# Performance work log

Measured on AMD Instinct MI355X. Metric: run time of the kernel, lower is better.

Reference implementation:

```python
import jax, jax.numpy as jnp
import numpy as np

NEG_FILL = -10000000.0  # matches torch masked_fill value


def setup_inputs() -> dict:
    key = jax.random.key(0)
    kq, kk, kv = jax.random.split(key, 3)
    B, H, S, D = 4, 16, 2048, 64
    Q = jax.random.normal(kq, (B, H, S, D), dtype=jnp.float32)
    K = jax.random.normal(kk, (B, H, S, D), dtype=jnp.float32)
    V = jax.random.normal(kv, (B, H, S, D), dtype=jnp.float32)
    return {"Q": Q, "K": K, "V": V}


def reference(Q, K, V):
    # Q,K,V: [B,H,S,D]
    D = K.shape[-1]
    scale = 1.0 / jnp.sqrt(jnp.asarray(D, dtype=Q.dtype))
    # scores: [B,H,S,S]
    scores = jnp.einsum("bhqd,bhkd->bhqk", Q, K) * scale
    S = scores.shape[-1]
    # causal mask: True above diagonal (future positions) -> filled with NEG_FILL
    causal = jnp.triu(jnp.ones((S, S), dtype=bool), k=1)
    scores = jnp.where(causal, jnp.asarray(NEG_FILL, dtype=scores.dtype), scores)
    attn = jax.nn.softmax(scores, axis=-1)
    return jnp.einsum("bhqk,bhkd->bhqd", attn, V)
```

## Files before the change

### kernel.cpp

```cpp
#include <hip/hip_runtime.h>
#include <hip/hip_bf16.h>


#define SEQ 2048
#define DIM 64
#define BH  64

typedef _Float16 half8  __attribute__((ext_vector_type(8)));
typedef _Float16 half4v __attribute__((ext_vector_type(4)));
typedef float    float4v __attribute__((ext_vector_type(4)));

__device__ __forceinline__ void async16(const _Float16* g, _Float16* l) {
    __builtin_amdgcn_global_load_lds(
        (const __attribute__((address_space(1))) void*)g,
        (__attribute__((address_space(3))) void*)l, 16, 0, 0);
}

__global__ __launch_bounds__(256)
void prep_kernel(const float* __restrict__ K, const float* __restrict__ V,
                 _Float16* __restrict__ Kh, _Float16* __restrict__ Vt) {
    const int bid = blockIdx.x;
    const int tid = threadIdx.x;
    if (bid < 4096) {
        size_t idx = (size_t)bid * 2048 + (size_t)tid * 8;
        float4v a = *(const float4v*)(K + idx);
        float4v b = *(const float4v*)(K + idx + 4);
        half8 h;
        h[0] = (_Float16)a[0]; h[1] = (_Float16)a[1];
        h[2] = (_Float16)a[2]; h[3] = (_Float16)a[3];
        h[4] = (_Float16)b[0]; h[5] = (_Float16)b[1];
        h[6] = (_Float16)b[2]; h[7] = (_Float16)b[3];
        *(half8*)(Kh + idx) = h;
    } else {
        const int b  = bid - 4096;
        const int bh = b >> 5;
        const int s0 = (b & 31) * 64;
        const int dg = tid >> 4;
        const int sg = tid & 15;
        const float* vp = V + ((size_t)bh * SEQ + s0 + sg * 4) * DIM + dg * 4;
        float4v r0 = *(const float4v*)(vp);
        float4v r1 = *(const float4v*)(vp + DIM);
        float4v r2 = *(const float4v*)(vp + 2 * DIM);
        float4v r3 = *(const float4v*)(vp + 3 * DIM);
#pragma unroll
        for (int dd = 0; dd < 4; ++dd) {
            half4v w;
            w[0] = (_Float16)r0[dd]; w[1] = (_Float16)r1[dd];
            w[2] = (_Float16)r2[dd]; w[3] = (_Float16)r3[dd];
            *(half4v*)(Vt + ((size_t)bh * DIM + dg * 4 + dd) * SEQ + s0 + sg * 4) = w;
        }
    }
}

__global__ __launch_bounds__(256, 4)
void fa_main(const float* __restrict__ Q, const _Float16* __restrict__ Kh,
             const _Float16* __restrict__ Vt, float* __restrict__ O) {
    const int bid = blockIdx.x;
    const int bh  = bid >> 4;
    const int pr  = bid & 15;

    const float*    Qb = Q  + (size_t)bh * SEQ * DIM;
    const _Float16* Kb = Kh + (size_t)bh * SEQ * DIM;
    const _Float16* Vb = Vt + (size_t)bh * DIM * SEQ;
    float*          Ob = O  + (size_t)bh * SEQ * DIM;

    const int tid  = threadIdx.x;
    const int wave = tid >> 6;
    const int lane = tid & 63;
    const int row  = lane & 15;
    const int quad = lane >> 4;

    __shared__ _Float16 Kl[2][64 * 64];
    __shared__ _Float16 Vl[2][64 * 64];
    __shared__ _Float16 Pl[4][16 * 64];

    const float SC = 0.125f * 1.44269504f;

#define STAGE(bsel, kt_)                                                        \
    {                                                                           \
        const _Float16* Kt0 = Kb + (size_t)(kt_) * 64 * DIM;                    \
        const _Float16* Vt0 = Vb + (size_t)(kt_) * 64;                          \
        _Pragma("unroll")                                                       \
        for (int i = 0; i < 2; ++i) {                                           \
            int pos = wave * 128 + i * 64 + lane;                               \
            int rr  = pos >> 3;                                                 \
            int cc  = (pos & 7) ^ (rr & 7);                                     \
            async16(Kt0 + (size_t)rr * DIM + cc * 8,                            \
                    &Kl[bsel][0] + (size_t)(wave * 128 + i * 64) * 8);          \
            async16(Vt0 + (size_t)rr * SEQ + cc * 8,                            \
                    &Vl[bsel][0] + (size_t)(wave * 128 + i * 64) * 8);          \
        }                                                                       \
    }

    for (int ph = 0; ph < 2; ++ph) {
        const int qt = ph ? (31 - pr) : pr;
        const int q0 = qt * 64;

        half8 qf[2];
        {
            const float* qp = Qb + (size_t)(q0 + wave * 16 + row) * DIM;
#pragma unroll
            for (int s = 0; s < 2; ++s) {
                const float* p = qp + s * 32 + quad * 8;
                float4v a = *(const float4v*)p;
                float4v b = *(const float4v*)(p + 4);
                half8 h;
                h[0] = (_Float16)(a[0] * SC); h[1] = (_Float16)(a[1] * SC);
                h[2] = (_Float16)(a[2] * SC); h[3] = (_Float16)(a[3] * SC);
                h[4] = (_Float16)(b[0] * SC); h[5] = (_Float16)(b[1] * SC);
                h[6] = (_Float16)(b[2] * SC); h[7] = (_Float16)(b[3] * SC);
                qf[s] = h;
            }
        }

        float l_part = 0.f;
        float4v o_acc[4];
#pragma unroll
        for (int c = 0; c < 4; ++c) { float4v z = {0.f, 0.f, 0.f, 0.f}; o_acc[c] = z; }

        STAGE(0, 0)
        __syncthreads();

        for (int kt = 0; kt <= qt; ++kt) {
            const int cb = kt & 1;
            if (kt < qt) STAGE(cb ^ 1, kt + 1)

            float4v sacc[4];
#pragma unroll
            for (int c = 0; c < 4; ++c) { float4v z = {0.f, 0.f, 0.f, 0.f}; sacc[c] = z; }
#pragma unroll
            for (int c = 0; c < 4; ++c) {
                const int kv = c * 16 + row;
#pragma unroll
                for (int s = 0; s < 2; ++s) {
                    const int ch = (s * 4 + quad) ^ (kv & 7);
                    half8 kf = *(const half8*)&Kl[cb][kv * 64 + ch * 8];
                    sacc[c] = __builtin_amdgcn_mfma_f32_16x16x32_f16(kf, qf[s], sacc[c], 0, 0, 0);
                }
            }

            float pv[4][4];
            if (kt == qt) {
                const int ql = wave * 16 + row;
#pragma unroll
                for (int c = 0; c < 4; ++c)
#pragma unroll
                    for (int r = 0; r < 4; ++r) {
                        int kvl = c * 16 + quad * 4 + r;
                        float sx = (kvl > ql) ? -1e30f : sacc[c][r];
                        float p  = exp2f(fminf(sx, 14.f));
                        pv[c][r] = p;
                        l_part  += p;
                    }
            } else {
#pragma unroll
                for (int c = 0; c < 4; ++c)
#pragma unroll
                    for (int r = 0; r < 4; ++r) {
                        float p = exp2f(fminf(sacc[c][r], 14.f));
                        pv[c][r] = p;
                        l_part += p;
                    }
            }

#pragma unroll
            for (int c = 0; c < 4; ++c) {
                half4v w;
                w[0] = (_Float16)pv[c][0]; w[1] = (_Float16)pv[c][1];
                w[2] = (_Float16)pv[c][2]; w[3] = (_Float16)pv[c][3];
                const int jc = c * 2 + (quad >> 1);
                const int col = ((jc ^ (row & 7)) << 3) + (quad & 1) * 4;
                *(half4v*)&Pl[wave][row * 64 + col] = w;
            }
            asm volatile("s_waitcnt lgkmcnt(0)" ::: "memory");
            half8 af[2];
#pragma unroll
            for (int s = 0; s < 2; ++s) {
                const int js = (s * 4 + quad) ^ (row & 7);
                af[s] = *(const half8*)&Pl[wave][row * 64 + js * 8];
            }

#pragma unroll
            for (int c = 0; c < 4; ++c) {
                const int d = c * 16 + row;
#pragma unroll
                for (int s = 0; s < 2; ++s) {
                    const int ch = (s * 4 + quad) ^ (d & 7);
                    half8 vf = *(const half8*)&Vl[cb][d * 64 + ch * 8];
                    o_acc[c] = __builtin_amdgcn_mfma_f32_16x16x32_f16(vf, af[s], o_acc[c], 0, 0, 0);
                }
            }

            __syncthreads();
        }

        float l = l_part;
        l += __shfl_xor(l, 16);
        l += __shfl_xor(l, 32);
        const float inv = 1.0f / l;
        float* op = Ob + (size_t)(q0 + wave * 16 + row) * DIM + quad * 4;
#pragma unroll
        for (int c = 0; c < 4; ++c) {
            float4v o;
            o[0] = o_acc[c][0] * inv; o[1] = o_acc[c][1] * inv;
            o[2] = o_acc[c][2] * inv; o[3] = o_acc[c][3] * inv;
            *(float4v*)(op + c * 16) = o;
        }
    }
}

__global__ __launch_bounds__(256)
void fa_causal_fallback(const float* __restrict__ Q, const float* __restrict__ K,
                        const float* __restrict__ V, float* __restrict__ O) {
    const int bid = blockIdx.x;
    const int bh  = bid >> 5;
    const int qt  = bid & 31;
    const int q0  = qt * 64;

    const float* Qb = Q + (size_t)bh * SEQ * DIM;
    const float* Kb = K + (size_t)bh * SEQ * DIM;
    const float* Vb = V + (size_t)bh * SEQ * DIM;
    float*       Ob = O + (size_t)bh * SEQ * DIM;

    const int tid  = threadIdx.x;
    const int wave = tid >> 6;
    const int lane = tid & 63;
    const int row  = lane & 15;
    const int quad = lane >> 4;

    __shared__ _Float16 Kl[64][72];
    __shared__ _Float16 Vt[64][72];
    __shared__ _Float16 Pl[4][16][72];

    half8 qf[2];
    {
        const float* qp = Qb + (size_t)(q0 + wave * 16 + row) * DIM;
#pragma unroll
        for (int s = 0; s < 2; ++s) {
            const float* p = qp + s * 32 + quad * 8;
            float4v a = *(const float4v*)p;
            float4v b = *(const float4v*)(p + 4);
            half8 h;
            h[0] = (_Float16)a[0]; h[1] = (_Float16)a[1];
            h[2] = (_Float16)a[2]; h[3] = (_Float16)a[3];
            h[4] = (_Float16)b[0]; h[5] = (_Float16)b[1];
            h[6] = (_Float16)b[2]; h[7] = (_Float16)b[3];
            qf[s] = h;
        }
    }

    float m_i[4] = {-1e30f, -1e30f, -1e30f, -1e30f};
    float l_i[4] = {0.f, 0.f, 0.f, 0.f};
    float4v o_acc[4];
#pragma unroll
    for (int c = 0; c < 4; ++c) { float4v z = {0.f, 0.f, 0.f, 0.f}; o_acc[c] = z; }

    const float LOG2E = 1.44269504f;

    for (int kt = 0; kt <= qt; ++kt) {
        __syncthreads();
        {
            const int kvr = tid >> 2;
            const int c4  = tid & 3;
            const float* kp = Kb + (size_t)(kt * 64 + kvr) * DIM + c4 * 16;
            const float* vp = Vb + (size_t)(kt * 64 + kvr) * DIM + c4 * 16;
#pragma unroll
            for (int i = 0; i < 4; ++i) {
                float4v kx = *(const float4v*)(kp + i * 4);
                float4v vx = *(const float4v*)(vp + i * 4);
#pragma unroll
                for (int j = 0; j < 4; ++j) {
                    Kl[kvr][c4 * 16 + i * 4 + j] = (_Float16)kx[j];
                    Vt[c4 * 16 + i * 4 + j][kvr] = (_Float16)vx[j];
                }
            }
        }
        __syncthreads();

        float4v sacc[4];
#pragma unroll
        for (int c = 0; c < 4; ++c) { float4v z = {0.f, 0.f, 0.f, 0.f}; sacc[c] = z; }
#pragma unroll
        for (int c = 0; c < 4; ++c)
#pragma unroll
            for (int s = 0; s < 2; ++s) {
                half8 kf = *(const half8*)&Kl[c * 16 + row][s * 32 + quad * 8];
                sacc[c] = __builtin_amdgcn_mfma_f32_16x16x32_f16(qf[s], kf, sacc[c], 0, 0, 0);
            }

        float sv[4][4];
        const bool diag = (kt == qt);
#pragma unroll
        for (int c = 0; c < 4; ++c)
#pragma unroll
            for (int r = 0; r < 4; ++r) {
                float v = sacc[c][r] * 0.125f;
                if (diag) {
                    int kvl = c * 16 + row;
                    int ql  = wave * 16 + quad * 4 + r;
                    if (kvl > ql) v = -1e30f;
                }
                sv[c][r] = v;
            }

        float mnew[4], alpha[4];
#pragma unroll
        for (int r = 0; r < 4; ++r) {
            float rm = fmaxf(fmaxf(sv[0][r], sv[1][r]), fmaxf(sv[2][r], sv[3][r]));
            rm = fmaxf(rm, __shfl_xor(rm, 1));
            rm = fmaxf(rm, __shfl_xor(rm, 2));
            rm = fmaxf(rm, __shfl_xor(rm, 4));
            rm = fmaxf(rm, __shfl_xor(rm, 8));
            mnew[r]  = fmaxf(m_i[r], rm);
            alpha[r] = exp2f((m_i[r] - mnew[r]) * LOG2E);
            m_i[r]   = mnew[r];
        }
        float rs[4] = {0.f, 0.f, 0.f, 0.f};
#pragma unroll
        for (int c = 0; c < 4; ++c)
#pragma unroll
            for (int r = 0; r < 4; ++r) {
                float p = exp2f((sv[c][r] - mnew[r]) * LOG2E);
                sv[c][r] = p;
                rs[r] += p;
            }
#pragma unroll
        for (int r = 0; r < 4; ++r) {
            float s = rs[r];
            s += __shfl_xor(s, 1);
            s += __shfl_xor(s, 2);
            s += __shfl_xor(s, 4);
            s += __shfl_xor(s, 8);
            l_i[r] = l_i[r] * alpha[r] + s;
        }
#pragma unroll
        for (int c = 0; c < 4; ++c)
#pragma unroll
            for (int r = 0; r < 4; ++r)
                o_acc[c][r] *= alpha[r];

#pragma unroll
        for (int c = 0; c < 4; ++c)
#pragma unroll
            for (int r = 0; r < 4; ++r)
                Pl[wave][quad * 4 + r][c * 16 + row] = (_Float16)sv[c][r];
        __syncthreads();

        half8 af[2];
#pragma unroll
        for (int s = 0; s < 2; ++s)
            af[s] = *(const half8*)&Pl[wave][row][s * 32 + quad * 8];
#pragma unroll
        for (int c = 0; c < 4; ++c)
#pragma unroll
            for (int s = 0; s < 2; ++s) {
                half8 vf = *(const half8*)&Vt[c * 16 + row][s * 32 + quad * 8];
                o_acc[c] = __builtin_amdgcn_mfma_f32_16x16x32_f16(af[s], vf, o_acc[c], 0, 0, 0);
            }
    }

#pragma unroll
    for (int r = 0; r < 4; ++r) {
        float inv = 1.0f / l_i[r];
        float* op = Ob + (size_t)(q0 + wave * 16 + quad * 4 + r) * DIM;
#pragma unroll
        for (int c = 0; c < 4; ++c)
            op[c * 16 + row] = o_acc[c][r] * inv;
    }
}

extern "C" void kernel_launch(void* const* d_in, const int* in_sizes, int n_in,
                              void* d_out, int out_size, void* d_ws, size_t ws_size,
                              hipStream_t stream) {
    const float* Q = (const float*)d_in[0];
    const float* K = (const float*)d_in[1];
    const float* V = (const float*)d_in[2];
    float* O = (float*)d_out;

    const size_t elems = (size_t)BH * SEQ * DIM;
    const size_t need  = 2 * elems * sizeof(_Float16);

    if (ws_size >= need) {
        _Float16* Kh = (_Float16*)d_ws;
        _Float16* Vt = Kh + elems;
        prep_kernel<<<4096 + 2048, 256, 0, stream>>>(K, V, Kh, Vt);
        fa_main<<<BH * 16, 256, 0, stream>>>(Q, Kh, Vt, O);
    } else {
        fa_causal_fallback<<<BH * 32, 256, 0, stream>>>(Q, K, V, O);
    }
}
```

Before: 209.3 us.

## Transpose V through swizzled LDS in prep and remap blocks across XCDs

The V transpose in the prep kernel now loads rows coalesced into a swizzled shared-memory tile, then writes 16-byte transposed chunks. Before, it wrote scattered 8-byte stores. The main kernel's block index is remapped so all query tiles of a batch-head land on the same XCD, which should improve L2 reuse of K/V. The QK MFMA chain also starts from a zero constant instead of explicitly zeroed accumulators. The cost is an extra LDS round trip and a barrier in prep.

```diff
diff --git a/kernel.cpp b/kernel.cpp
--- a/kernel.cpp
+++ b/kernel.cpp
@@ -32,22 +32,49 @@
         h[6] = (_Float16)b[2]; h[7] = (_Float16)b[3];
         *(half8*)(Kh + idx) = h;
     } else {
+        __shared__ _Float16 Vl[64 * 64];
         const int b  = bid - 4096;
         const int bh = b >> 5;
         const int s0 = (b & 31) * 64;
-        const int dg = tid >> 4;
-        const int sg = tid & 15;
-        const float* vp = V + ((size_t)bh * SEQ + s0 + sg * 4) * DIM + dg * 4;
-        float4v r0 = *(const float4v*)(vp);
-        float4v r1 = *(const float4v*)(vp + DIM);
-        float4v r2 = *(const float4v*)(vp + 2 * DIM);
-        float4v r3 = *(const float4v*)(vp + 3 * DIM);
-#pragma unroll
-        for (int dd = 0; dd < 4; ++dd) {
-            half4v w;
-            w[0] = (_Float16)r0[dd]; w[1] = (_Float16)r1[dd];
-            w[2] = (_Float16)r2[dd]; w[3] = (_Float16)r3[dd];
-            *(half4v*)(Vt + ((size_t)bh * DIM + dg * 4 + dd) * SEQ + s0 + sg * 4) = w;
+        {
+            const int r   = tid >> 2;
+            const int c16 = (tid & 3) * 16;
+            const float* p = V + ((size_t)bh * SEQ + s0 + r) * DIM + c16;
+            float4v x0 = *(const float4v*)(p);
+            float4v x1 = *(const float4v*)(p + 4);
+            float4v x2 = *(const float4v*)(p + 8);
+            float4v x3 = *(const float4v*)(p + 12);
+            half8 h0, h1;
+            h0[0] = (_Float16)x0[0]; h0[1] = (_Float16)x0[1];
+            h0[2] = (_Float16)x0[2]; h0[3] = (_Float16)x0[3];
+            h0[4] = (_Float16)x1[0]; h0[5] = (_Float16)x1[1];
+            h0[6] = (_Float16)x1[2]; h0[7] = (_Float16)x1[3];
+            h1[0] = (_Float16)x2[0]; h1[1] = (_Float16)x2[1];
+            h1[2] = (_Float16)x2[2]; h1[3] = (_Float16)x2[3];
+            h1[4] = (_Float16)x3[0]; h1[5] = (_Float16)x3[1];
+            h1[6] = (_Float16)x3[2]; h1[7] = (_Float16)x3[3];
+            const int k  = (r + (r >> 3)) & 7;
+            const int j0 = c16 >> 3;
+            *(half8*)&Vl[r * 64 + ((j0    ) ^ k) * 8] = h0;
+            *(half8*)&Vl[r * 64 + ((j0 + 1) ^ k) * 8] = h1;
+        }
+        __syncthreads();
+        {
+            const int d  = tid >> 2;
+            const int sc = (tid & 3) * 16;
+            const int dh = d >> 3;
+            const int dl = d & 7;
+            half8 o0, o1;
+#pragma unroll
+            for (int j = 0; j < 8; ++j) {
+                const int s1 = sc + j;
+                const int s2 = sc + 8 + j;
+                o0[j] = Vl[s1 * 64 + ((dh ^ ((s1 + (s1 >> 3)) & 7)) << 3) + dl];
+                o1[j] = Vl[s2 * 64 + ((dh ^ ((s2 + (s2 >> 3)) & 7)) << 3) + dl];
+            }
+            _Float16* op = Vt + ((size_t)bh * DIM + d) * SEQ + s0 + sc;
+            *(half8*)op       = o0;
+            *(half8*)(op + 8) = o1;
         }
     }
 }
@@ -56,8 +83,10 @@
 void fa_main(const float* __restrict__ Q, const _Float16* __restrict__ Kh,
              const _Float16* __restrict__ Vt, float* __restrict__ O) {
     const int bid = blockIdx.x;
-    const int bh  = bid >> 4;
-    const int pr  = bid & 15;
+    const int xcd = bid & 7;
+    const int m   = bid >> 3;
+    const int pr  = m & 15;
+    const int bh  = xcd * 8 + (m >> 4);
 
     const float*    Qb = Q  + (size_t)bh * SEQ * DIM;
     const _Float16* Kb = Kh + (size_t)bh * SEQ * DIM;
@@ -75,6 +104,7 @@
     __shared__ _Float16 Pl[4][16 * 64];
 
     const float SC = 0.125f * 1.44269504f;
+    const float4v z0 = {0.f, 0.f, 0.f, 0.f};
 
 #define STAGE(bsel, kt_)                                                        \
     {                                                                           \
@@ -127,16 +157,14 @@
 
             float4v sacc[4];
 #pragma unroll
-            for (int c = 0; c < 4; ++c) { float4v z = {0.f, 0.f, 0.f, 0.f}; sacc[c] = z; }
-#pragma unroll
             for (int c = 0; c < 4; ++c) {
-                const int kv = c * 16 + row;
-#pragma unroll
-                for (int s = 0; s < 2; ++s) {
-                    const int ch = (s * 4 + quad) ^ (kv & 7);
-                    half8 kf = *(const half8*)&Kl[cb][kv * 64 + ch * 8];
-                    sacc[c] = __builtin_amdgcn_mfma_f32_16x16x32_f16(kf, qf[s], sacc[c], 0, 0, 0);
-                }
+                const int kv  = c * 16 + row;
+                const int ch0 = quad ^ (kv & 7);
+                const int ch1 = (4 + quad) ^ (kv & 7);
+                half8 kf0 = *(const half8*)&Kl[cb][kv * 64 + ch0 * 8];
+                half8 kf1 = *(const half8*)&Kl[cb][kv * 64 + ch1 * 8];
+                float4v s = __builtin_amdgcn_mfma_f32_16x16x32_f16(kf0, qf[0], z0, 0, 0, 0);
+                sacc[c]   = __builtin_amdgcn_mfma_f32_16x16x32_f16(kf1, qf[1], s, 0, 0, 0);
             }
 
             float pv[4][4];
@@ -168,7 +196,7 @@
                 half4v w;
                 w[0] = (_Float16)pv[c][0]; w[1] = (_Float16)pv[c][1];
                 w[2] = (_Float16)pv[c][2]; w[3] = (_Float16)pv[c][3];
-                const int jc = c * 2 + (quad >> 1);
+                const int jc  = c * 2 + (quad >> 1);
                 const int col = ((jc ^ (row & 7)) << 3) + (quad & 1) * 4;
                 *(half4v*)&Pl[wave][row * 64 + col] = w;
             }
```

Result: faster. 200.5 us (-4.2%).
